# Optimization experiments

Measured on AMD Instinct MI355X. Metric: run time of the kernel, lower is better.

Reference implementation:

```python
import jax, jax.numpy as jnp
import numpy as np

DIM = 1024
HEADS = 16
HEAD_DIM = DIM // HEADS
DFF = 4 * DIM
BASE_THETA, K_DOP, K_NOR, K_SERO = 0.5, 0.2, 0.15, 0.1
EPS = 1e-5


def _layernorm(x, g, b):
    mu = jnp.mean(x, axis=-1, keepdims=True)
    var = jnp.var(x, axis=-1, keepdims=True)
    return (x - mu) * jax.lax.rsqrt(var + EPS) * g + b


def setup_inputs() -> dict:
    key = jax.random.key(0)
    ks = jax.random.split(key, 16)
    s = 0.02
    d = {
        'x': jax.random.normal(ks[0], (2, 2048, DIM), dtype=jnp.float32),
        'ln1_g': jnp.ones((DIM,), jnp.float32),
        'ln1_b': jnp.zeros((DIM,), jnp.float32),
        'qkv_w': jax.random.normal(ks[1], (DIM, 3 * DIM), jnp.float32) * s,
        'qkv_b': jnp.zeros((3 * DIM,), jnp.float32),
        'proj_w': jax.random.normal(ks[2], (DIM, DIM), jnp.float32) * s,
        'proj_b': jnp.zeros((DIM,), jnp.float32),
        'kq_w': jax.random.normal(ks[3], (DIM, DIM), jnp.float32) * s,
        'kq_b': jnp.zeros((DIM,), jnp.float32),
        'kk_w': jax.random.normal(ks[4], (DIM, DIM), jnp.float32) * s,
        'kk_b': jnp.zeros((DIM,), jnp.float32),
        'kv_w': jax.random.normal(ks[5], (DIM, DIM), jnp.float32) * s,
        'kv_b': jnp.zeros((DIM,), jnp.float32),
        'ko_w': jax.random.normal(ks[6], (DIM, DIM), jnp.float32) * s,
        'ko_b': jnp.zeros((DIM,), jnp.float32),
        'ln2_g': jnp.ones((DIM,), jnp.float32),
        'ln2_b': jnp.zeros((DIM,), jnp.float32),
        'fc1_w': jax.random.normal(ks[7], (DIM, DFF), jnp.float32) * s,
        'fc1_b': jnp.zeros((DFF,), jnp.float32),
        'fc2_w': jax.random.normal(ks[8], (DFF, DIM), jnp.float32) * s,
        'fc2_b': jnp.zeros((DIM,), jnp.float32),
    }
    return d


def _mha(x, qkv_w, qkv_b, proj_w, proj_b):
    B, N, C = x.shape
    qkv = (x @ qkv_w + qkv_b).reshape(B, N, 3, HEADS, HEAD_DIM)
    q, k, v = qkv[:, :, 0], qkv[:, :, 1], qkv[:, :, 2]  # [B,N,H,Hd]
    scale = HEAD_DIM ** -0.5
    attn = jnp.einsum('bnhd,bmhd->bhnm', q, k) * scale
    attn = jax.nn.softmax(attn, axis=-1)
    out = jnp.einsum('bhnm,bmhd->bnhd', attn, v).reshape(B, N, C)
    return out @ proj_w + proj_b


def _kernel_attn(x, kq_w, kq_b, kk_w, kk_b, kv_w, kv_b, ko_w, ko_b):
    q = x @ kq_w + kq_b
    k = x @ kk_w + kk_b
    v = x @ kv_w + kv_b
    qk = jnp.einsum('bnc,bmc->bnm', q, k)
    theta = (BASE_THETA + K_DOP * jax.nn.sigmoid(qk)
             + K_NOR * jnp.tanh(qk) + K_SERO * jax.nn.relu(qk))
    attn = jax.nn.softmax(theta, axis=-1)
    out = jnp.einsum('bnm,bmc->bnc', attn, v)
    return out @ ko_w + ko_b


def reference(x, ln1_g, ln1_b, qkv_w, qkv_b, proj_w, proj_b,
              kq_w, kq_b, kk_w, kk_b, kv_w, kv_b, ko_w, ko_b,
              ln2_g, ln2_b, fc1_w, fc1_b, fc2_w, fc2_b):
    x = x + _mha(_layernorm(x, ln1_g, ln1_b), qkv_w, qkv_b, proj_w, proj_b)
    x = x + _kernel_attn(x, kq_w, kq_b, kk_w, kk_b, kv_w, kv_b, ko_w, ko_b)
    h = _layernorm(x, ln2_g, ln2_b)
    h = jax.nn.gelu(h @ fc1_w + fc1_b, approximate=False) @ fc2_w + fc2_b
    return x + h
```

## Files before the change

### kernel.cpp

```cpp
#include <hip/hip_runtime.h>
#include <math.h>


#define DIMC   1024
#define NTOK   4096
#define SEQ    2048
#define NHEADS 16
#define DFFC   4096

typedef unsigned short u16;
typedef __attribute__((ext_vector_type(8))) short s16x8;
typedef __attribute__((ext_vector_type(4))) float f32x4;
#define MFMA16(a,b,c) __builtin_amdgcn_mfma_f32_16x16x32_bf16(a,b,c,0,0,0)

__device__ __forceinline__ float b2f(u16 u){ return __uint_as_float(((unsigned int)u)<<16); }
__device__ __forceinline__ u16 f2b(float f){
  unsigned int u = __float_as_uint(f);
  u += 0x7fffu + ((u>>16)&1u);
  return (u16)(u>>16);
}

__device__ __forceinline__ float ldIn(const void* base, long idx, int f32){
  return f32 ? ((const float*)base)[idx] : b2f(((const u16*)base)[idx]);
}
__device__ __forceinline__ float4 ldIn4(const void* base, long idx, int f32){
  if (f32) return *(const float4*)((const float*)base + idx);
  ushort4 u = *(const ushort4*)((const u16*)base + idx);
  return make_float4(b2f(u.x), b2f(u.y), b2f(u.z), b2f(u.w));
}
__device__ __forceinline__ void ld8(const void* base, long idx, int f32, float* v){
  if (f32){
    float4 a = *(const float4*)((const float*)base + idx);
    float4 b = *(const float4*)((const float*)base + idx + 4);
    v[0]=a.x; v[1]=a.y; v[2]=a.z; v[3]=a.w;
    v[4]=b.x; v[5]=b.y; v[6]=b.z; v[7]=b.w;
  } else {
    ushort4 a = *(const ushort4*)((const u16*)base + idx);
    ushort4 b = *(const ushort4*)((const u16*)base + idx + 4);
    v[0]=b2f(a.x); v[1]=b2f(a.y); v[2]=b2f(a.z); v[3]=b2f(a.w);
    v[4]=b2f(b.x); v[5]=b2f(b.y); v[6]=b2f(b.z); v[7]=b2f(b.w);
  }
}
__device__ __forceinline__ void st8(void* base, long idx, int f32, const float* v){
  if (f32){
    *(float4*)((float*)base + idx)     = make_float4(v[0],v[1],v[2],v[3]);
    *(float4*)((float*)base + idx + 4) = make_float4(v[4],v[5],v[6],v[7]);
  } else {
    unsigned int q0 = (unsigned int)f2b(v[0]) | ((unsigned int)f2b(v[1])<<16);
    unsigned int q1 = (unsigned int)f2b(v[2]) | ((unsigned int)f2b(v[3])<<16);
    unsigned int q2 = (unsigned int)f2b(v[4]) | ((unsigned int)f2b(v[5])<<16);
    unsigned int q3 = (unsigned int)f2b(v[6]) | ((unsigned int)f2b(v[7])<<16);
    *(uint4*)((u16*)base + idx) = make_uint4(q0,q1,q2,q3);
  }
}

__device__ __forceinline__ float waveSum(float v){
  #pragma unroll
  for (int off=32; off>0; off>>=1) v += __shfl_xor(v, off, 64);
  return v;
}

__device__ __forceinline__ void async16(const u16* g, u16* l){
  __builtin_amdgcn_global_load_lds(
      (const __attribute__((address_space(1))) unsigned int*)g,
      (__attribute__((address_space(3))) unsigned int*)l, 16, 0, 0);
}

__global__ void detect_kernel(const void* ones, int* flag){
  if (threadIdx.x == 0 && blockIdx.x == 0){
    unsigned int w = *(const unsigned int*)ones;
    *flag = (w == 0x3F803F80u) ? 0 : 1;
  }
}

__global__ __launch_bounds__(256)
void transpose_w(const void* __restrict__ in, u16* __restrict__ out,
                 const int* __restrict__ flagp, int K, int N)
{
  __shared__ u16 t[32][36];
  const int fl = *flagp;
  const int n0 = blockIdx.x*32, k0 = blockIdx.y*32;
  const int tx = threadIdx.x & 31, ty = threadIdx.x >> 5;
  #pragma unroll
  for (int r = ty; r < 32; r += 8)
    t[r][tx] = f2b(ldIn(in, (long)(k0+r)*N + n0 + tx, fl));
  __syncthreads();
  #pragma unroll
  for (int r = ty; r < 32; r += 8)
    out[(long)(n0+r)*K + k0 + tx] = t[tx][r];
}

__global__ __launch_bounds__(256)
void transpose_b(const u16* __restrict__ in, u16* __restrict__ out,
                 int K, int N, long sIn, long sOut)
{
  __shared__ u16 t[32][36];
  const long zi = (long)blockIdx.z*sIn, zo = (long)blockIdx.z*sOut;
  const int n0 = blockIdx.x*32, k0 = blockIdx.y*32;
  const int tx = threadIdx.x & 31, ty = threadIdx.x >> 5;
  #pragma unroll
  for (int r = ty; r < 32; r += 8)
    t[r][tx] = in[zi + (long)(k0+r)*N + n0 + tx];
  __syncthreads();
  #pragma unroll
  for (int r = ty; r < 32; r += 8)
    out[zo + (long)(n0+r)*K + k0 + tx] = t[tx][r];
}

__global__ __launch_bounds__(256)
void conv_bf16(const void* __restrict__ in, u16* __restrict__ out,
               const int* __restrict__ flagp)
{
  const int fl = *flagp;
  long i = ((long)blockIdx.x*256 + threadIdx.x)*4;
  float4 v = ldIn4(in, i, fl);
  ushort4 o; o.x=f2b(v.x); o.y=f2b(v.y); o.z=f2b(v.z); o.w=f2b(v.w);
  *(ushort4*)(out+i) = o;
}

template<int BM, int MODE, int ACT>
__global__ __launch_bounds__(256)
void gemm_mfma(const u16* __restrict__ A, const u16* __restrict__ BT,
               const void* __restrict__ bias, const void* __restrict__ bias2,
               const void* __restrict__ bias3, const void* res,
               void* C, u16* Cv, const int* __restrict__ flagp, int cExt,
               int M, int N, int K, int lda, int ldb, int ldc,
               long sA, long sB, long sC)
{
  constexpr int BUFS = (BM+128)*64;
  constexpr int ST   = BM*132;
  constexpr int LSZ  = (3*BUFS > ST) ? 3*BUFS : ST;
  __shared__ u16 lds[LSZ];

  const int fl = *flagp;
  const int fC = cExt ? fl : 0;
  const int z = blockIdx.z;
  A += (long)z*sA; BT += (long)z*sB;
  const long coff = (long)z*sC;
  const int m0 = blockIdx.x*BM, n0 = blockIdx.y*128;
  const int tid = threadIdx.x, w = tid>>6, l = tid&63;
  const int lr = l&15, lq = l>>4;
  constexpr int FM = BM/32;
  constexpr int NIA = BM/32;
  const int wm = (w&1)*(BM/2), wn = (w>>1)*64;

  const int rq = l>>3;
  const int cperm = (l&7) ^ rq;
  const u16* pa = A  + (long)(m0 + rq)*lda + cperm*8;
  const u16* pb = BT + (long)(n0 + rq)*ldb + cperm*8;

  f32x4 acc[FM][4];
  #pragma unroll
  for (int i=0;i<FM;i++)
    #pragma unroll
    for (int j=0;j<4;j++) acc[i][j] = (f32x4){0.f,0.f,0.f,0.f};

  auto stage = [&](u16* buf){
    u16* As = buf;
    u16* Bs = buf + BM*64;
    #pragma unroll
    for (int p=0;p<NIA;p++){
      const int ia = p*4 + w;
      async16(pa + (long)ia*8*lda, &As[ia*512]);
    }
    #pragma unroll
    for (int p=0;p<4;p++){
      const int ib = p*4 + w;
      async16(pb + (long)ib*8*ldb, &Bs[ib*512]);
    }
    pa += 64; pb += 64;
  };

  auto compute = [&](const u16* As){
    const u16* Bs = As + BM*64;
    const int swz = lr & 7;
    #pragma unroll
    for (int h=0; h<2; h++){
      s16x8 af[FM], bf[4];
      const int slot = ((h*4 + lq) ^ swz) << 3;
      #pragma unroll
      for (int i=0;i<FM;i++)
        af[i] = *(const s16x8*)&As[(wm + i*16 + lr)*64 + slot];
      #pragma unroll
      for (int j=0;j<4;j++)
        bf[j] = *(const s16x8*)&Bs[(wn + j*16 + lr)*64 + slot];
      __builtin_amdgcn_s_setprio(1);
      #pragma unroll
      for (int i=0;i<FM;i++)
        #pragma unroll
        for (int j=0;j<4;j++) acc[i][j] = MFMA16(af[i], bf[j], acc[i][j]);
      __builtin_amdgcn_s_setprio(0);
    }
  };

  auto waitL = [&](){
    if constexpr (BM==128) asm volatile("s_waitcnt vmcnt(8)" ::: "memory");
    else                   asm volatile("s_waitcnt vmcnt(6)" ::: "memory");
    __builtin_amdgcn_s_barrier();
  };

  const int nk = K >> 6;
  stage(lds);
  stage(lds + BUFS);

  int cur = 0;
  for (int t = 0; t < nk-2; ++t){
    waitL();
    int nxt = cur+2; if (nxt >= 3) nxt -= 3;
    stage(lds + nxt*BUFS);
    compute(lds + cur*BUFS);
    cur = (cur==2) ? 0 : cur+1;
  }
  waitL();
  compute(lds + cur*BUFS);
  cur = (cur==2) ? 0 : cur+1;
  asm volatile("s_waitcnt vmcnt(0)" ::: "memory");
  __builtin_amdgcn_s_barrier();
  compute(lds + cur*BUFS);
  __syncthreads();

  #pragma unroll
  for (int i=0;i<FM;i++)
    #pragma unroll
    for (int j=0;j<4;j++)
      #pragma unroll
      for (int r=0;r<4;r++)
        lds[(wm + i*16 + lq*4 + r)*132 + wn + j*16 + lr] = f2b(acc[i][j][r]);
  __syncthreads();

  const int trow = tid >> 4, tcol = (tid & 15)*8;
  const int gcol = n0 + tcol;
  #pragma unroll
  for (int p=0; p<BM/16; p++){
    const int row = p*16 + trow;
    const long grow = m0 + row;
    float v[8];
    #pragma unroll
    for (int e=0;e<8;e++) v[e] = b2f(lds[row*132 + tcol + e]);

    if (MODE == 2){
      #pragma unroll
      for (int e=0;e<8;e++){
        float q = v[e];
        float sig = 1.f/(1.f+__expf(-q));
        float th  = 1.f - 2.f/(__expf(2.f*q)+1.f);
        v[e] = __expf(0.5f + 0.2f*sig + 0.15f*th + 0.1f*fmaxf(q,0.f));
      }
      st8(C, coff + grow*ldc + gcol, 0, v);
    } else if (MODE == 1){
      if (n0 < 2048){
        const void* bb = (n0 < 1024) ? bias : bias2;
        const int cofs = (n0 < 1024) ? 0 : 1024;
        float bv[8]; ld8(bb, gcol - cofs, fl, bv);
        #pragma unroll
        for (int e=0;e<8;e++) v[e] += bv[e];
        st8(C, grow*2048 + gcol, 0, v);
      } else {
        float bv[8]; ld8(bias3, gcol - 2048, fl, bv);
        #pragma unroll
        for (int e=0;e<8;e++) v[e] += bv[e];
        st8(Cv, grow*1024 + (gcol - 2048), 0, v);
      }
    } else {
      if (bias){
        float bv[8]; ld8(bias, gcol, fl, bv);
        #pragma unroll
        for (int e=0;e<8;e++) v[e] += bv[e];
      }
      if (ACT==1){
        #pragma unroll
        for (int e=0;e<8;e++){
          float u = v[e];
          float y = 1.5957691216f*u*(1.f + 0.044715f*u*u);
          v[e] = u / (1.f + __expf(-y));
        }
      }
      const long idx = coff + grow*ldc + gcol;
      if (res){
        float rv[8]; ld8(res, idx, fl, rv);
        #pragma unroll
        for (int e=0;e<8;e++) v[e] += rv[e];
      }
      st8(C, idx, fC, v);
    }
  }
}

__global__ __launch_bounds__(256)
void ln_kernel(const void* __restrict__ in, const void* __restrict__ g,
               const void* __restrict__ b, u16* __restrict__ outp,
               const int* __restrict__ flagp, int inFlagged)
{
  const int fl = *flagp;
  const int fin = inFlagged ? fl : 0;
  const int row = blockIdx.x;
  const int tid = threadIdx.x;
  float4 xv = ldIn4(in, (long)row*DIMC + tid*4, fin);
  float v0=xv.x, v1=xv.y, v2=xv.z, v3=xv.w;
  float s  = v0+v1+v2+v3;
  float s2 = v0*v0+v1*v1+v2*v2+v3*v3;
  s = waveSum(s); s2 = waveSum(s2);
  __shared__ float sh[8];
  int w = tid>>6, ln = tid&63;
  if (ln==0){ sh[w]=s; sh[4+w]=s2; }
  __syncthreads();
  float ts  = sh[0]+sh[1]+sh[2]+sh[3];
  float ts2 = sh[4]+sh[5]+sh[6]+sh[7];
  float mu  = ts * (1.f/1024.f);
  float var = ts2 * (1.f/1024.f) - mu*mu;
  float rs  = rsqrtf(var + 1e-5f);
  int c = tid*4;
  float4 gv = ldIn4(g, c, fl);
  float4 bv = ldIn4(b, c, fl);
  ushort4 o;
  o.x = f2b((v0-mu)*rs*gv.x + bv.x);
  o.y = f2b((v1-mu)*rs*gv.y + bv.y);
  o.z = f2b((v2-mu)*rs*gv.z + bv.z);
  o.w = f2b((v3-mu)*rs*gv.w + bv.w);
  *(ushort4*)(outp + (long)row*DIMC + c) = o;
}

__global__ __launch_bounds__(256)
void mha_flash(const u16* __restrict__ qkv, u16* __restrict__ outp)
{
  __shared__ u16 Kl[64][72];
  __shared__ u16 Vt[64][72];
  __shared__ u16 Pl[4][16][72];
  const int h  = blockIdx.y;
  const int bb = blockIdx.z;
  const int q0 = blockIdx.x * 64;
  const int tid = threadIdx.x, lane = tid & 63, w = tid >> 6;
  const int lr = lane & 15, lq = lane >> 4;
  const long tokBase = (long)bb * SEQ;

  s16x8 qf0, qf1;
  {
    const u16* qp = qkv + (tokBase + q0 + w*16 + lr)*3072 + h*64 + lq*8;
    qf0 = *(const s16x8*)qp;
    qf1 = *(const s16x8*)(qp + 32);
  }
  f32x4 o[4];
  #pragma unroll
  for (int d=0;d<4;d++) o[d] = (f32x4){0.f,0.f,0.f,0.f};
  float lsum[4] = {0.f,0.f,0.f,0.f};

  const int p2 = tid & 31, dg = tid >> 5;

  for (int k0 = 0; k0 < SEQ; k0 += 64){
    __syncthreads();
    #pragma unroll
    for (int c=0;c<2;c++){
      int idx = tid + c*256;
      int key = idx >> 3, d0 = (idx & 7) * 8;
      *(uint4*)&Kl[key][d0] =
        *(const uint4*)(qkv + (tokBase + k0 + key)*3072 + 1024 + h*64 + d0);
    }
    {
      const u16* vsrc = qkv + (tokBase + k0 + 2*p2)*3072 + 2048 + h*64 + dg*8;
      ushort4 a0 = *(const ushort4*)vsrc,        a1 = *(const ushort4*)(vsrc+4);
      ushort4 b0 = *(const ushort4*)(vsrc+3072), b1 = *(const ushort4*)(vsrc+3076);
      unsigned int pk;
      #pragma unroll
      for (int jj=0;jj<4;jj++){
        pk = ((const u16*)&a0)[jj] | ((unsigned int)((const u16*)&b0)[jj] << 16);
        *(unsigned int*)&Vt[dg*8+jj][2*p2] = pk;
        pk = ((const u16*)&a1)[jj] | ((unsigned int)((const u16*)&b1)[jj] << 16);
        *(unsigned int*)&Vt[dg*8+4+jj][2*p2] = pk;
      }
    }
    __syncthreads();

    f32x4 s[4];
    #pragma unroll
    for (int c=0;c<4;c++){
      s[c] = (f32x4){0.f,0.f,0.f,0.f};
      s16x8 kf0 = *(const s16x8*)&Kl[c*16+lr][lq*8];
      s16x8 kf1 = *(const s16x8*)&Kl[c*16+lr][lq*8+32];
      s[c] = MFMA16(qf0, kf0, s[c]);
      s[c] = MFMA16(qf1, kf1, s[c]);
    }
    #pragma unroll
    for (int c=0;c<4;c++)
      #pragma unroll
      for (int r=0;r<4;r++){
        float pp = __expf(s[c][r]*0.125f);
        lsum[r] += pp;
        Pl[w][lq*4+r][c*16+lr] = f2b(pp);
      }
    s16x8 pf0 = *(const s16x8*)&Pl[w][lr][lq*8];
    s16x8 pf1 = *(const s16x8*)&Pl[w][lr][32+lq*8];
    #pragma unroll
    for (int d=0;d<4;d++){
      s16x8 vf0 = *(const s16x8*)&Vt[d*16+lr][lq*8];
      s16x8 vf1 = *(const s16x8*)&Vt[d*16+lr][32+lq*8];
      o[d] = MFMA16(pf0, vf0, o[d]);
      o[d] = MFMA16(pf1, vf1, o[d]);
    }
  }

  #pragma unroll
  for (int r=0;r<4;r++){
    float lv = lsum[r];
    #pragma unroll
    for (int off=1; off<16; off<<=1) lv += __shfl_xor(lv, off, 64);
    float inv = 1.f / lv;
    long row = (tokBase + q0 + w*16 + lq*4 + r) * (long)DIMC + h*64;
    outp[row + lr     ] = f2b(o[0][r]*inv);
    outp[row + lr + 16] = f2b(o[1][r]*inv);
    outp[row + lr + 32] = f2b(o[2][r]*inv);
    outp[row + lr + 48] = f2b(o[3][r]*inv);
  }
}

__global__ __launch_bounds__(256)
void norm_kernel(const u16* __restrict__ S, u16* __restrict__ kout)
{
  const int row = blockIdx.x;
  const int tid = threadIdx.x;
  const u16* Sr = S + (long)(row>>11)*4194304 + (long)(row&2047)*2048;
  ushort4 u0 = *(const ushort4*)(Sr + tid*8);
  ushort4 u1 = *(const ushort4*)(Sr + tid*8 + 4);
  float s = b2f(u0.x)+b2f(u0.y)+b2f(u0.z)+b2f(u0.w)
          + b2f(u1.x)+b2f(u1.y)+b2f(u1.z)+b2f(u1.w);
  s = waveSum(s);
  __shared__ float sh[4];
  int w = tid>>6, ln = tid&63;
  if (ln==0) sh[w]=s;
  __syncthreads();
  float inv = 1.f/(sh[0]+sh[1]+sh[2]+sh[3]);
  u16* orow = kout + (long)row*DIMC;
  ushort4 v = *(ushort4*)(orow + tid*4);
  v.x = f2b(b2f(v.x)*inv); v.y = f2b(b2f(v.y)*inv);
  v.z = f2b(b2f(v.z)*inv); v.w = f2b(b2f(v.w)*inv);
  *(ushort4*)(orow + tid*4) = v;
}

extern "C" void kernel_launch(void* const* d_in, const int* in_sizes, int n_in,
                              void* d_out, int out_size, void* d_ws, size_t ws_size,
                              hipStream_t stream)
{
  const void* x      = d_in[0];
  const void* ln1_g  = d_in[1];
  const void* ln1_b  = d_in[2];
  const void* qkv_w  = d_in[3];
  const void* qkv_b  = d_in[4];
  const void* proj_w = d_in[5];
  const void* proj_b = d_in[6];
  const void* kq_w   = d_in[7];
  const void* kq_b   = d_in[8];
  const void* kk_w   = d_in[9];
  const void* kk_b   = d_in[10];
  const void* kv_w   = d_in[11];
  const void* kv_b   = d_in[12];
  const void* ko_w   = d_in[13];
  const void* ko_b   = d_in[14];
  const void* ln2_g  = d_in[15];
  const void* ln2_b  = d_in[16];
  const void* fc1_w  = d_in[17];
  const void* fc1_b  = d_in[18];
  const void* fc2_w  = d_in[19];
  const void* fc2_b  = d_in[20];

  int* flag = (int*)d_ws;
  u16* Ar   = (u16*)((char*)d_ws + 64);
  u16* B0   = Ar + 4194304L;
  u16* QK   = B0;
  u16* Vt   = B0 + 8388608L;
  u16* C0   = B0 + 12582912L;
  u16* Sb   = C0;
  u16* WT   = C0;
  u16* vtmp = C0 + 4194304L;
  u16* WT2  = C0 + 4194304L;
  u16* FC1  = B0;
  u16* Qr   = B0;

  dim3 blk(256);
  const void* np = nullptr;

  detect_kernel<<<1, 64, 0, stream>>>(ln1_g, flag);
  transpose_w<<<dim3(96,32), blk, 0, stream>>>(qkv_w, WT, flag, DIMC, 3*DIMC);
  ln_kernel<<<NTOK, blk, 0, stream>>>(x, ln1_g, ln1_b, Ar, flag, 1);
  gemm_mfma<64,0,0><<<dim3(64,24,1), blk, 0, stream>>>(
      Ar, WT, qkv_b, np, np, np, Qr, nullptr, flag, 0,
      NTOK, 3*DIMC, DIMC, DIMC, DIMC, 3*DIMC, 0,0,0);
  mha_flash<<<dim3(SEQ/64, NHEADS, 2), blk, 0, stream>>>(Qr, Ar);
  transpose_w<<<dim3(32,32), blk, 0, stream>>>(proj_w, WT, flag, DIMC, DIMC);
  gemm_mfma<64,0,0><<<dim3(64,8,1), blk, 0, stream>>>(
      Ar, WT, proj_b, np, np, x, d_out, nullptr, flag, 1,
      NTOK, DIMC, DIMC, DIMC, DIMC, DIMC, 0,0,0);
  conv_bf16<<<NTOK, blk, 0, stream>>>(d_out, Ar, flag);
  transpose_w<<<dim3(32,32), blk, 0, stream>>>(kq_w, WT,            flag, DIMC, DIMC);
  transpose_w<<<dim3(32,32), blk, 0, stream>>>(kk_w, WT + 1048576L, flag, DIMC, DIMC);
  transpose_w<<<dim3(32,32), blk, 0, stream>>>(kv_w, WT + 2097152L, flag, DIMC, DIMC);
  gemm_mfma<64,1,0><<<dim3(64,24,1), blk, 0, stream>>>(
      Ar, WT, kq_b, kk_b, kv_b, np, QK, vtmp, flag, 0,
      NTOK, 3*DIMC, DIMC, DIMC, DIMC, 2048, 0,0,0);
  transpose_b<<<dim3(32,64,2), blk, 0, stream>>>(
      vtmp, Vt, SEQ, DIMC, 2097152L, 2097152L);
  gemm_mfma<64,2,0><<<dim3(32,16,2), blk, 0, stream>>>(
      QK, QK + 1024, np, np, np, np, Sb, nullptr, flag, 0,
      SEQ, SEQ, DIMC, 2048, 2048, SEQ, 4194304L, 4194304L, 4194304L);
  gemm_mfma<64,0,0><<<dim3(32,8,2), blk, 0, stream>>>(
      Sb, Vt, np, np, np, np, Ar, nullptr, flag, 0,
      SEQ, DIMC, SEQ, SEQ, SEQ, DIMC, 4194304L, 2097152L, 2097152L);
  norm_kernel<<<NTOK, blk, 0, stream>>>(Sb, Ar);
  transpose_w<<<dim3(32,32), blk, 0, stream>>>(ko_w, WT, flag, DIMC, DIMC);
  gemm_mfma<64,0,0><<<dim3(64,8,1), blk, 0, stream>>>(
      Ar, WT, ko_b, np, np, d_out, d_out, nullptr, flag, 1,
      NTOK, DIMC, DIMC, DIMC, DIMC, DIMC, 0,0,0);
  ln_kernel<<<NTOK, blk, 0, stream>>>(d_out, ln2_g, ln2_b, Ar, flag, 1);
  transpose_w<<<dim3(128,32), blk, 0, stream>>>(fc1_w, WT2, flag, DIMC, DFFC);
  gemm_mfma<64,0,1><<<dim3(64,32,1), blk, 0, stream>>>(
      Ar, WT2, fc1_b, np, np, np, FC1, nullptr, flag, 0,
      NTOK, DFFC, DIMC, DIMC, DIMC, DFFC, 0,0,0);
  transpose_w<<<dim3(32,128), blk, 0, stream>>>(fc2_w, WT2, flag, DFFC, DIMC);
  gemm_mfma<64,0,0><<<dim3(64,8,1), blk, 0, stream>>>(
      FC1, WT2, fc2_b, np, np, d_out, d_out, nullptr, flag, 1,
      NTOK, DIMC, DFFC, DFFC, DFFC, DIMC, 0,0,0);
}
```

Measured before the change: 640.0 us.

## Use 128-row GEMM tiles with double buffering, prefetch K/V in flash attention

Switches the large GEMMs (QKV, kernel-attn projections, QK scores, FC1) to 128-row tiles, using a two-buffer LDS pipeline so the bigger tile still fits in shared memory. The QKV GEMM gains a new mode that folds the softmax scale and log2(e) into Q, so the flash-attention kernel can call exp2f directly. Flash attention now prefetches the next K/V tile into registers while the current one is used, and packs pairs of P values with a lane shuffle for 32-bit LDS stores. Bigger tiles raise data reuse but halve the block count and cut occupancy, and the two-buffer pipeline adds an extra barrier per k-step.

```diff
diff --git a/kernel.cpp b/kernel.cpp
--- a/kernel.cpp
+++ b/kernel.cpp
@@ -7,6 +7,7 @@
 #define SEQ    2048
 #define NHEADS 16
 #define DFFC   4096
+#define QSCALE 0.1803368801f
 
 typedef unsigned short u16;
 typedef __attribute__((ext_vector_type(8))) short s16x8;
@@ -127,9 +128,10 @@
                int M, int N, int K, int lda, int ldb, int ldc,
                long sA, long sB, long sC)
 {
+  constexpr int DEPTH = (BM==128) ? 2 : 3;
   constexpr int BUFS = (BM+128)*64;
   constexpr int ST   = BM*132;
-  constexpr int LSZ  = (3*BUFS > ST) ? 3*BUFS : ST;
+  constexpr int LSZ  = (DEPTH*BUFS > ST) ? DEPTH*BUFS : ST;
   __shared__ u16 lds[LSZ];
 
   const int fl = *flagp;
@@ -193,31 +195,47 @@
     }
   };
 
-  auto waitL = [&](){
-    if constexpr (BM==128) asm volatile("s_waitcnt vmcnt(8)" ::: "memory");
-    else                   asm volatile("s_waitcnt vmcnt(6)" ::: "memory");
-    __builtin_amdgcn_s_barrier();
-  };
-
   const int nk = K >> 6;
-  stage(lds);
-  stage(lds + BUFS);
-
-  int cur = 0;
-  for (int t = 0; t < nk-2; ++t){
+
+  if constexpr (DEPTH == 3){
+    auto waitL = [&](){
+      asm volatile("s_waitcnt vmcnt(6)" ::: "memory");
+      __builtin_amdgcn_s_barrier();
+    };
+    stage(lds);
+    stage(lds + BUFS);
+    int cur = 0;
+    for (int t = 0; t < nk-2; ++t){
+      waitL();
+      int nxt = cur+2; if (nxt >= 3) nxt -= 3;
+      stage(lds + nxt*BUFS);
+      compute(lds + cur*BUFS);
+      cur = (cur==2) ? 0 : cur+1;
+    }
     waitL();
-    int nxt = cur+2; if (nxt >= 3) nxt -= 3;
-    stage(lds + nxt*BUFS);
     compute(lds + cur*BUFS);
     cur = (cur==2) ? 0 : cur+1;
-  }
-  waitL();
-  compute(lds + cur*BUFS);
-  cur = (cur==2) ? 0 : cur+1;
-  asm volatile("s_waitcnt vmcnt(0)" ::: "memory");
-  __builtin_amdgcn_s_barrier();
-  compute(lds + cur*BUFS);
-  __syncthreads();
+    asm volatile("s_waitcnt vmcnt(0)" ::: "memory");
+    __builtin_amdgcn_s_barrier();
+    compute(lds + cur*BUFS);
+    __syncthreads();
+  } else {
+    stage(lds);
+    stage(lds + BUFS);
+    int cur = 0;
+    for (int t = 0; t < nk-1; ++t){
+      asm volatile("s_waitcnt vmcnt(8)" ::: "memory");
+      __builtin_amdgcn_s_barrier();
+      compute(lds + cur*BUFS);
+      __syncthreads();
+      if (t+2 < nk) stage(lds + cur*BUFS);
+      cur ^= 1;
+    }
+    asm volatile("s_waitcnt vmcnt(0)" ::: "memory");
+    __builtin_amdgcn_s_barrier();
+    compute(lds + cur*BUFS);
+    __syncthreads();
+  }
 
   #pragma unroll
   for (int i=0;i<FM;i++)
@@ -266,6 +284,10 @@
         float bv[8]; ld8(bias, gcol, fl, bv);
         #pragma unroll
         for (int e=0;e<8;e++) v[e] += bv[e];
+      }
+      if (MODE == 3 && gcol < 1024){
+        #pragma unroll
+        for (int e=0;e<8;e++) v[e] *= QSCALE;
       }
       if (ACT==1){
         #pragma unroll
@@ -345,29 +367,39 @@
   float lsum[4] = {0.f,0.f,0.f,0.f};
 
   const int p2 = tid & 31, dg = tid >> 5;
-
+  const int kk = tid >> 3, kd = (tid & 7) * 8;
+
+  uint4 kr0, kr1;
+  ushort4 va0, va1, vb0, vb1;
+  const u16* kbase = qkv + (tokBase + kk)*3072 + 1024 + h*64 + kd;
+  const u16* vbase = qkv + (tokBase + 2*p2)*3072 + 2048 + h*64 + dg*8;
+
+  auto ldKV = [&](int k0){
+    const u16* kp = kbase + (long)k0*3072;
+    kr0 = *(const uint4*)kp;
+    kr1 = *(const uint4*)(kp + 32*3072);
+    const u16* vp = vbase + (long)k0*3072;
+    va0 = *(const ushort4*)vp;          va1 = *(const ushort4*)(vp+4);
+    vb0 = *(const ushort4*)(vp+3072);   vb1 = *(const ushort4*)(vp+3076);
+  };
+  auto wrKV = [&](){
+    *(uint4*)&Kl[kk][kd]      = kr0;
+    *(uint4*)&Kl[32+kk][kd]   = kr1;
+    unsigned int pk;
+    #pragma unroll
+    for (int jj=0;jj<4;jj++){
+      pk = ((const u16*)&va0)[jj] | ((unsigned int)((const u16*)&vb0)[jj] << 16);
+      *(unsigned int*)&Vt[dg*8+jj][2*p2] = pk;
+      pk = ((const u16*)&va1)[jj] | ((unsigned int)((const u16*)&vb1)[jj] << 16);
+      *(unsigned int*)&Vt[dg*8+4+jj][2*p2] = pk;
+    }
+  };
+
+  ldKV(0);
   for (int k0 = 0; k0 < SEQ; k0 += 64){
     __syncthreads();
-    #pragma unroll
-    for (int c=0;c<2;c++){
-      int idx = tid + c*256;
-      int key = idx >> 3, d0 = (idx & 7) * 8;
-      *(uint4*)&Kl[key][d0] =
-        *(const uint4*)(qkv + (tokBase + k0 + key)*3072 + 1024 + h*64 + d0);
-    }
-    {
-      const u16* vsrc = qkv + (tokBase + k0 + 2*p2)*3072 + 2048 + h*64 + dg*8;
-      ushort4 a0 = *(const ushort4*)vsrc,        a1 = *(const ushort4*)(vsrc+4);
-      ushort4 b0 = *(const ushort4*)(vsrc+3072), b1 = *(const ushort4*)(vsrc+3076);
-      unsigned int pk;
-      #pragma unroll
-      for (int jj=0;jj<4;jj++){
-        pk = ((const u16*)&a0)[jj] | ((unsigned int)((const u16*)&b0)[jj] << 16);
-        *(unsigned int*)&Vt[dg*8+jj][2*p2] = pk;
-        pk = ((const u16*)&a1)[jj] | ((unsigned int)((const u16*)&b1)[jj] << 16);
-        *(unsigned int*)&Vt[dg*8+4+jj][2*p2] = pk;
-      }
-    }
+    wrKV();
+    if (k0 + 64 < SEQ) ldKV(k0 + 64);
     __syncthreads();
 
     f32x4 s[4];
@@ -383,9 +415,12 @@
     for (int c=0;c<4;c++)
       #pragma unroll
       for (int r=0;r<4;r++){
-        float pp = __expf(s[c][r]*0.125f);
+        float pp = exp2f(s[c][r]);
         lsum[r] += pp;
-        Pl[w][lq*4+r][c*16+lr] = f2b(pp);
+        unsigned int pb = (unsigned int)f2b(pp);
+        unsigned int nb = (unsigned int)__shfl_xor((int)pb, 1, 64);
+        if ((lr & 1) == 0)
+          *(unsigned int*)&Pl[w][lq*4+r][c*16+lr] = pb | (nb << 16);
       }
     s16x8 pf0 = *(const s16x8*)&Pl[w][lr][lq*8];
     s16x8 pf1 = *(const s16x8*)&Pl[w][lr][32+lq*8];
@@ -480,7 +515,7 @@
   detect_kernel<<<1, 64, 0, stream>>>(ln1_g, flag);
   transpose_w<<<dim3(96,32), blk, 0, stream>>>(qkv_w, WT, flag, DIMC, 3*DIMC);
   ln_kernel<<<NTOK, blk, 0, stream>>>(x, ln1_g, ln1_b, Ar, flag, 1);
-  gemm_mfma<64,0,0><<<dim3(64,24,1), blk, 0, stream>>>(
+  gemm_mfma<128,3,0><<<dim3(32,24,1), blk, 0, stream>>>(
       Ar, WT, qkv_b, np, np, np, Qr, nullptr, flag, 0,
       NTOK, 3*DIMC, DIMC, DIMC, DIMC, 3*DIMC, 0,0,0);
   mha_flash<<<dim3(SEQ/64, NHEADS, 2), blk, 0, stream>>>(Qr, Ar);
@@ -492,12 +527,12 @@
   transpose_w<<<dim3(32,32), blk, 0, stream>>>(kq_w, WT,            flag, DIMC, DIMC);
   transpose_w<<<dim3(32,32), blk, 0, stream>>>(kk_w, WT + 1048576L, flag, DIMC, DIMC);
   transpose_w<<<dim3(32,32), blk, 0, stream>>>(kv_w, WT + 2097152L, flag, DIMC, DIMC);
-  gemm_mfma<64,1,0><<<dim3(64,24,1), blk, 0, stream>>>(
+  gemm_mfma<128,1,0><<<dim3(32,24,1), blk, 0, stream>>>(
       Ar, WT, kq_b, kk_b, kv_b, np, QK, vtmp, flag, 0,
       NTOK, 3*DIMC, DIMC, DIMC, DIMC, 2048, 0,0,0);
   transpose_b<<<dim3(32,64,2), blk, 0, stream>>>(
       vtmp, Vt, SEQ, DIMC, 2097152L, 2097152L);
-  gemm_mfma<64,2,0><<<dim3(32,16,2), blk, 0, stream>>>(
+  gemm_mfma<128,2,0><<<dim3(16,16,2), blk, 0, stream>>>(
       QK, QK + 1024, np, np, np, np, Sb, nullptr, flag, 0,
       SEQ, SEQ, DIMC, 2048, 2048, SEQ, 4194304L, 4194304L, 4194304L);
   gemm_mfma<64,0,0><<<dim3(32,8,2), blk, 0, stream>>>(
@@ -510,7 +545,7 @@
       NTOK, DIMC, DIMC, DIMC, DIMC, DIMC, 0,0,0);
   ln_kernel<<<NTOK, blk, 0, stream>>>(d_out, ln2_g, ln2_b, Ar, flag, 1);
   transpose_w<<<dim3(128,32), blk, 0, stream>>>(fc1_w, WT2, flag, DIMC, DFFC);
-  gemm_mfma<64,0,1><<<dim3(64,32,1), blk, 0, stream>>>(
+  gemm_mfma<128,0,1><<<dim3(32,32,1), blk, 0, stream>>>(
       Ar, WT2, fc1_b, np, np, np, FC1, nullptr, flag, 0,
       NTOK, DFFC, DIMC, DIMC, DIMC, DFFC, 0,0,0);
   transpose_w<<<dim3(32,128), blk, 0, stream>>>(fc2_w, WT2, flag, DFFC, DIMC);
```

Measured after the change: 644.0 us. No clear change (+0.6%).
